# Optimization experiments

Hardware: AMD Instinct MI355X
Metric: run time of the kernel (lower is better)

## Reference

```python
import jax, jax.numpy as jnp
import numpy as np

B = 32768
T = 30
H = 384


def setup_inputs() -> dict:
    key = jax.random.key(0)
    ks = jax.random.split(key, 16)

    def lin(k, out_d, in_d):
        # torch nn.Linear init: U(-1/sqrt(in_d), 1/sqrt(in_d))
        bound = 1.0 / np.sqrt(in_d)
        kw, kb = jax.random.split(k)
        W = jax.random.uniform(kw, (out_d, in_d), jnp.float32, -bound, bound)
        b = jax.random.uniform(kb, (out_d,), jnp.float32, -bound, bound)
        return W, b

    Wp, bp = lin(ks[0], 128, 3)        # plan_input
    Ws, bs = lin(ks[1], 128, 3)        # state_input
    # GRUCell params: weight_ih [3H,128], weight_hh [3H,H], init U(-1/sqrt(H),..)
    gb = 1.0 / np.sqrt(H)
    W_ih = jax.random.uniform(ks[2], (3 * H, 128), jnp.float32, -gb, gb)
    b_ih = jax.random.uniform(ks[3], (3 * H,), jnp.float32, -gb, gb)
    W_hh = jax.random.uniform(ks[4], (3 * H, H), jnp.float32, -gb, gb)
    b_hh = jax.random.uniform(ks[5], (3 * H,), jnp.float32, -gb, gb)
    Wd1, bd1 = lin(ks[6], 64, H)       # decode Linear(384,64)
    Wd2, bd2 = lin(ks[7], 3, 64)       # decode Linear(64,3)

    init_hidden = jax.random.normal(ks[8], (B, H), jnp.float32)
    plan = jax.random.normal(ks[9], (B, T, 3), jnp.float32)
    gate = jax.random.uniform(ks[10], (B, 1), jnp.float32)
    init_state = jax.random.normal(ks[11], (B, 3), jnp.float32)

    return {
        "init_hidden": init_hidden, "plan": plan, "gate": gate,
        "init_state": init_state,
        "Wp": Wp, "bp": bp, "Ws": Ws, "bs": bs,
        "W_ih": W_ih, "b_ih": b_ih, "W_hh": W_hh, "b_hh": b_hh,
        "Wd1": Wd1, "bd1": bd1, "Wd2": Wd2, "bd2": bd2,
    }


def reference(init_hidden, plan, gate, init_state,
              Wp, bp, Ws, bs, W_ih, b_ih, W_hh, b_hh,
              Wd1, bd1, Wd2, bd2):
    # Dropout(0.1) is identity in eval mode.
    plan_seq = jnp.swapaxes(plan[:, :T, :3], 0, 1)  # [T,B,3]

    def step(carry, plan_t):
        hidden, state = carry  # [B,H], [B,3]
        x = (state @ Ws.T + bs) + (plan_t @ Wp.T + bp) * gate  # [B,128]
        gi = x @ W_ih.T + b_ih          # [B,3H]
        gh = hidden @ W_hh.T + b_hh     # [B,3H]
        ir, iz, inn = jnp.split(gi, 3, axis=-1)
        hr, hz, hn = jnp.split(gh, 3, axis=-1)
        r = jax.nn.sigmoid(ir + hr)
        z = jax.nn.sigmoid(iz + hz)
        n = jnp.tanh(inn + r * hn)
        hidden = (1.0 - z) * n + z * hidden
        dec = jax.nn.elu(hidden @ Wd1.T + bd1) @ Wd2.T + bd2  # [B,3]
        state = dec + state
        return (hidden, state), state

    _, outs = jax.lax.scan(step, (init_hidden, init_state[:, :3]), plan_seq)
    return jnp.swapaxes(outs, 0, 1)  # [B,T,3]
```

## Files before the change

### kernel.cpp

```cpp
#include <hip/hip_runtime.h>


#define TT  30
#define NPH 50
#define PHU 12288
#define HS  392

typedef unsigned short u16;
typedef __bf16 bf16x8 __attribute__((ext_vector_type(8)));
typedef u16    u16x8  __attribute__((ext_vector_type(8)));
typedef float  f32x16 __attribute__((ext_vector_type(16)));

__device__ __forceinline__ u16 f2b(float f){
  unsigned u = __float_as_uint(f);
  u += 0x7FFFu + ((u >> 16) & 1u);
  return (u16)(u >> 16);
}
__device__ __forceinline__ float b2f(u16 h){ return __uint_as_float(((unsigned)h) << 16); }

__device__ __forceinline__ f32x16 mfma32(u16x8 a, u16x8 b, f32x16 c){
  return __builtin_amdgcn_mfma_f32_32x32x16_bf16(
      __builtin_bit_cast(bf16x8, a), __builtin_bit_cast(bf16x8, b), c, 0, 0, 0);
}
__device__ __forceinline__ void lds_fence(){ asm volatile("s_waitcnt lgkmcnt(0)" ::: "memory"); }
__device__ __forceinline__ void vm_fence(){ asm volatile("s_waitcnt vmcnt(0)" ::: "memory"); }
__device__ __forceinline__ float sigf(float x){ return __builtin_amdgcn_rcpf(1.f + __expf(-x)); }
__device__ __forceinline__ float tanh_(float x){ return 2.f*__builtin_amdgcn_rcpf(1.f + __expf(-2.f*x)) - 1.f; }

__device__ __forceinline__ void stage16(const u16* g, u16* l){
  __builtin_amdgcn_global_load_lds(
      (const __attribute__((address_space(1))) unsigned int*)g,
      (__attribute__((address_space(3))) unsigned int*)l, 16, 0, 0);
}

__global__ void prep_kernel(const float* __restrict__ Wih, const float* __restrict__ Whh,
                            const float* __restrict__ Wd1, const float* __restrict__ Wd2,
                            const float* __restrict__ bih, const float* __restrict__ bhh,
                            const float* __restrict__ Ws,  const float* __restrict__ bs,
                            const float* __restrict__ Wp,  const float* __restrict__ bp,
                            u16* __restrict__ stream, u16* __restrict__ wd2p,
                            u16* __restrict__ wxp, float* __restrict__ gb)
{
  int i = blockIdx.x*blockDim.x + threadIdx.x;
  if (i < 442368){
    int row = i/384, k = i - row*384;
    int g = row/384, unit = row - g*384, c = unit>>5, lc = unit&31;
    int kf = k>>4, hl = (k>>3)&1, j = k&7;
    int phase = c*4 + 1 + g;
    stream[(size_t)phase*PHU + kf*512 + (lc+32*hl)*8 + j] = f2b(Whh[i]);
  }
  if (i < 147456){
    int row = i>>7, k = i&127;
    int g = row/384, unit = row - g*384, c = unit>>5, lc = unit&31;
    int kf = k>>4, hl = (k>>3)&1, j = k&7;
    int phase = c*4;
    stream[(size_t)phase*PHU + (g*8+kf)*512 + (lc+32*hl)*8 + j] = f2b(Wih[i]);
  }
  if (i < 24576){
    int row = i/384, k = i - row*384;
    int ct = row>>5, lc = row&31;
    int kf = k>>4, hl = (k>>3)&1, j = k&7;
    int phase = 48 + ct;
    stream[(size_t)phase*PHU + kf*512 + (lc+32*hl)*8 + j] = f2b(Wd1[i]);
  }
  if (i < 2048){
    int kf = i>>9, r = i&511;
    int n = (r>>3)&31, hl = r>>8, j = r&7;
    int k = kf*16 + hl*8 + j;
    wd2p[i] = f2b((n<3) ? Wd2[n*64 + k] : 0.f);
  }
  if (i < 2048){
    int tl = i>>9, r = i&511;
    int n = (r>>3)&31, hl = r>>8, j = r&7;
    int k = hl*8 + j, u = tl*32 + n;
    float v = 0.f;
    if      (k <= 2) v = Ws[u*3 + k];
    else if (k == 3) v = bs[u];
    else if (k <= 6) v = Wp[u*3 + (k-4)];
    else if (k == 7) v = bp[u];
    wxp[i] = f2b(v);
  }
  if (i < 384){
    gb[i*4+0] = bih[i]       + bhh[i];
    gb[i*4+1] = bih[384+i]   + bhh[384+i];
    gb[i*4+2] = bih[768+i];
    gb[i*4+3] = bhh[768+i];
  }
}

__global__ __launch_bounds__(256, 1)
void gru_main(const float* __restrict__ ih, const float* __restrict__ plan,
              const float* __restrict__ gate, const float* __restrict__ istate,
              const u16* __restrict__ stream, const u16* __restrict__ wd2p,
              const u16* __restrict__ wxp, const float* __restrict__ gb,
              const float* __restrict__ bd1, const float* __restrict__ bd2,
              float* __restrict__ out)
{
  __shared__ __attribute__((aligned(16))) u16 wb[2][PHU];
  __shared__ __attribute__((aligned(16))) u16 hn[4][32*HS];
  __shared__ float sst[4][32][4];

  const int tid  = threadIdx.x;
  const int wave = tid >> 6, lane = tid & 63;
  const int m    = lane & 31, hl = lane >> 5;
  const int R0   = blockIdx.x*128 + wave*32;
  u16* hw = hn[wave];

  const float gt    = gate[R0 + m];
  const float bd1v0 = bd1[m], bd1v1 = bd1[32+m];
  const float bd2v  = (m<3) ? bd2[m] : 0.f;

  if (lane < 32){
    const float* sp = istate + (size_t)(R0+lane)*3;
    sst[wave][lane][0]=sp[0]; sst[wave][lane][1]=sp[1];
    sst[wave][lane][2]=sp[2]; sst[wave][lane][3]=0.f;
  }

  u16x8 hold[24];
#pragma unroll
  for (int kf=0; kf<24; ++kf){
    const float* p = ih + (size_t)(R0+m)*384 + kf*16 + hl*8;
    float4 a = *(const float4*)p;
    float4 b = *(const float4*)(p+4);
    u16x8 v;
    v[0]=f2b(a.x); v[1]=f2b(a.y); v[2]=f2b(a.z); v[3]=f2b(a.w);
    v[4]=f2b(b.x); v[5]=f2b(b.y); v[6]=f2b(b.z); v[7]=f2b(b.w);
    hold[kf]=v;
    *(u16x8*)&hw[m*HS + kf*16 + hl*8] = v;
  }

  const u16* srcb = stream + wave*3072 + lane*8;
  auto stage = [&](int ph, int bsel){
    const u16* s = srcb + (size_t)ph*PHU;
    u16* d = &wb[bsel][wave*3072];
#pragma unroll
    for (int ii=0; ii<6; ++ii) stage16(s + ii*512, d + ii*512);
  };

  stage(0, 0);
  vm_fence(); __syncthreads();
  int buf = 0, gp = 0;

#pragma unroll 1
  for (int t=0; t<TT; ++t){
    u16x8 a8;
    {
      float4 sv = *(const float4*)&sst[wave][m][0];
      const float* pp = plan + (size_t)(R0+m)*(TT*3) + t*3;
      float f0=sv.x, f1=sv.y, f2=sv.z, f3=1.f;
      float f4=gt*pp[0], f5=gt*pp[1], f6=gt*pp[2], f7=gt;
      if (hl){ a8[0]=0;a8[1]=0;a8[2]=0;a8[3]=0;a8[4]=0;a8[5]=0;a8[6]=0;a8[7]=0; }
      else { a8[0]=f2b(f0);a8[1]=f2b(f1);a8[2]=f2b(f2);a8[3]=f2b(f3);
             a8[4]=f2b(f4);a8[5]=f2b(f5);a8[6]=f2b(f6);a8[7]=f2b(f7); }
    }
    u16x8 xf[8];
#pragma unroll
    for (int tl=0; tl<4; ++tl){
      f32x16 ax;
#pragma unroll
      for (int r=0;r<16;++r) ax[r]=0.f;
      ax = mfma32(a8, *(const u16x8*)(wxp + tl*512 + lane*8), ax);
#pragma unroll
      for (int r=0;r<16;++r){
        int row = (r&3) + ((r>>2)<<3) + 4*hl;
        hw[row*HS + m] = f2b(ax[r]);
      }
      lds_fence();
      xf[2*tl]   = *(const u16x8*)&hw[m*HS + hl*8];
      xf[2*tl+1] = *(const u16x8*)&hw[m*HS + 16 + hl*8];
      lds_fence();
    }
    *(u16x8*)&hw[m*HS + hl*8]      = hold[0];
    *(u16x8*)&hw[m*HS + 16 + hl*8] = hold[1];
    lds_fence();

#pragma unroll 1
    for (int c=0; c<12; ++c){
      f32x16 aR, aZ, aNI, aNH;
      {
        const float4 b4 = *(const float4*)(gb + (size_t)(c*32+m)*4);
#pragma unroll
        for (int r=0;r<16;++r){ aR[r]=b4.x; aZ[r]=b4.y; aNI[r]=b4.z; aNH[r]=b4.w; }
      }
      {
        int np = gp+1; stage(np, buf^1);
        const u16* W = wb[buf];
#pragma unroll
        for (int kf=0; kf<8; ++kf){
          u16x8 bR = *(const u16x8*)(W + (kf    )*512 + lane*8);
          u16x8 bZ = *(const u16x8*)(W + (8+kf  )*512 + lane*8);
          u16x8 bN = *(const u16x8*)(W + (16+kf )*512 + lane*8);
          aR  = mfma32(xf[kf], bR, aR);
          aZ  = mfma32(xf[kf], bZ, aZ);
          aNI = mfma32(xf[kf], bN, aNI);
        }
        vm_fence(); __syncthreads(); buf^=1; gp=np;
      }
      {
        int np = gp+1; stage(np, buf^1);
        const u16* W = wb[buf];
#pragma unroll
        for (int kf=0; kf<24; ++kf)
          aR = mfma32(hold[kf], *(const u16x8*)(W + kf*512 + lane*8), aR);
        vm_fence(); __syncthreads(); buf^=1; gp=np;
      }
      {
        int np = gp+1; stage(np, buf^1);
        const u16* W = wb[buf];
#pragma unroll
        for (int kf=0; kf<24; ++kf)
          aZ = mfma32(hold[kf], *(const u16x8*)(W + kf*512 + lane*8), aZ);
        vm_fence(); __syncthreads(); buf^=1; gp=np;
      }
      {
        int np = gp+1; stage(np, buf^1);
        const u16* W = wb[buf];
#pragma unroll
        for (int kf=0; kf<24; ++kf)
          aNH = mfma32(hold[kf], *(const u16x8*)(W + kf*512 + lane*8), aNH);
#pragma unroll
        for (int r=0;r<16;++r){
          int row = (r&3) + ((r>>2)<<3) + 4*hl;
          float rr = sigf(aR[r]);
          float zz = sigf(aZ[r]);
          float nn = tanh_(aNI[r] + rr*aNH[r]);
          int off = row*HS + c*32 + m;
          float ho = b2f(hw[off]);
          hw[off] = f2b((1.f-zz)*nn + zz*ho);
        }
        vm_fence(); __syncthreads(); buf^=1; gp=np;
      }
    }

    lds_fence();
#pragma unroll
    for (int kf=0; kf<24; ++kf)
      hold[kf] = *(const u16x8*)&hw[m*HS + kf*16 + hl*8];

    f32x16 a0, a1;
#pragma unroll
    for (int r=0;r<16;++r){ a0[r]=bd1v0; a1[r]=bd1v1; }
    {
      int np = gp+1; stage(np, buf^1);
      const u16* W = wb[buf];
#pragma unroll
      for (int kf=0; kf<24; ++kf)
        a0 = mfma32(hold[kf], *(const u16x8*)(W + kf*512 + lane*8), a0);
      vm_fence(); __syncthreads(); buf^=1; gp=np;
    }
    {
      int np = (gp+1 == NPH) ? 0 : gp+1;
      stage(np, buf^1);
      const u16* W = wb[buf];
#pragma unroll
      for (int kf=0; kf<24; ++kf)
        a1 = mfma32(hold[kf], *(const u16x8*)(W + kf*512 + lane*8), a1);

      u16x8 wd2f0 = *(const u16x8*)(wd2p + 0*512 + lane*8);
      u16x8 wd2f1 = *(const u16x8*)(wd2p + 1*512 + lane*8);
      u16x8 wd2f2 = *(const u16x8*)(wd2p + 2*512 + lane*8);
      u16x8 wd2f3 = *(const u16x8*)(wd2p + 3*512 + lane*8);

      f32x16 ao;
#pragma unroll
      for (int r=0;r<16;++r) ao[r]=0.f;
#pragma unroll
      for (int r=0;r<16;++r){
        int row = (r&3) + ((r>>2)<<3) + 4*hl;
        float e = a0[r]; e = e>0.f ? e : (__expf(e)-1.f);
        hw[row*HS + m] = f2b(e);
      }
      lds_fence();
      {
        u16x8 af0 = *(const u16x8*)&hw[m*HS + hl*8];
        u16x8 af1 = *(const u16x8*)&hw[m*HS + 16 + hl*8];
        ao = mfma32(af0, wd2f0, ao);
        ao = mfma32(af1, wd2f1, ao);
      }
      lds_fence();
#pragma unroll
      for (int r=0;r<16;++r){
        int row = (r&3) + ((r>>2)<<3) + 4*hl;
        float e = a1[r]; e = e>0.f ? e : (__expf(e)-1.f);
        hw[row*HS + m] = f2b(e);
      }
      lds_fence();
      {
        u16x8 af0 = *(const u16x8*)&hw[m*HS + hl*8];
        u16x8 af1 = *(const u16x8*)&hw[m*HS + 16 + hl*8];
        ao = mfma32(af0, wd2f2, ao);
        ao = mfma32(af1, wd2f3, ao);
      }
      lds_fence();
      *(u16x8*)&hw[m*HS + hl*8]      = hold[0];
      *(u16x8*)&hw[m*HS + 16 + hl*8] = hold[1];

#pragma unroll
      for (int r=0;r<16;++r){
        int row = (r&3) + ((r>>2)<<3) + 4*hl;
        if (m < 3){
          float ns = sst[wave][row][m] + ao[r] + bd2v;
          out[(size_t)(R0+row)*(TT*3) + t*3 + m] = ns;
          sst[wave][row][m] = ns;
        }
      }
      vm_fence(); __syncthreads(); buf^=1; gp=np;
    }
  }
}

extern "C" void kernel_launch(void* const* d_in, const int* in_sizes, int n_in,
                              void* d_out, int out_size, void* d_ws, size_t ws_size,
                              hipStream_t stream)
{
  (void)in_sizes; (void)n_in; (void)out_size; (void)ws_size;
  const float* ih     = (const float*)d_in[0];
  const float* plan   = (const float*)d_in[1];
  const float* gatep  = (const float*)d_in[2];
  const float* istate = (const float*)d_in[3];
  const float* Wp     = (const float*)d_in[4];
  const float* bp     = (const float*)d_in[5];
  const float* Ws     = (const float*)d_in[6];
  const float* bs     = (const float*)d_in[7];
  const float* Wih    = (const float*)d_in[8];
  const float* bih    = (const float*)d_in[9];
  const float* Whh    = (const float*)d_in[10];
  const float* bhh    = (const float*)d_in[11];
  const float* Wd1    = (const float*)d_in[12];
  const float* bd1    = (const float*)d_in[13];
  const float* Wd2    = (const float*)d_in[14];
  const float* bd2    = (const float*)d_in[15];

  u16*   wstream = (u16*)d_ws;
  u16*   wd2p    = (u16*)((char*)d_ws + 1228800);
  u16*   wxp     = (u16*)((char*)d_ws + 1232896);
  float* gb      = (float*)((char*)d_ws + 1236992);

  prep_kernel<<<1728, 256, 0, stream>>>(Wih, Whh, Wd1, Wd2, bih, bhh, Ws, bs, Wp, bp,
                                        wstream, wd2p, wxp, gb);
  gru_main<<<256, 256, 0, stream>>>(ih, plan, gatep, istate,
                                    wstream, wd2p, wxp, gb, bd1, bd2, (float*)d_out);
}
```

Baseline: 1.727 ms.

## Split hidden columns across wave pairs to double waves per block

Each group of 32 rows is now handled by a pair of waves, each computing half of the 384 hidden units, with the weight stream relaid into per-role half phases. Block size doubles to 512 threads so more waves hide MFMA and LDS latency, and per-wave work per phase is halved. The cost is twice as many block barriers per timestep and cross-wave exchange of hidden state and decode activations through LDS; register pressure under the new launch bounds may also rise.

```diff
diff --git a/kernel.cpp b/kernel.cpp
--- a/kernel.cpp
+++ b/kernel.cpp
@@ -2,8 +2,9 @@
 
 
 #define TT  30
-#define NPH 50
-#define PHU 12288
+#define NHP 50
+#define SPU 12288
+#define RHU 6144
 #define HS  392
 
 typedef unsigned short u16;
@@ -46,22 +47,27 @@
     int row = i/384, k = i - row*384;
     int g = row/384, unit = row - g*384, c = unit>>5, lc = unit&31;
     int kf = k>>4, hl = (k>>3)&1, j = k&7;
-    int phase = c*4 + 1 + g;
-    stream[(size_t)phase*PHU + kf*512 + (lc+32*hl)*8 + j] = f2b(Whh[i]);
+    int role = c/6, ci = c - role*6;
+    int q = ci*96 + 24 + g*24 + kf;
+    int sp = q/12, f = q - sp*12;
+    stream[(size_t)sp*SPU + role*RHU + f*512 + (lc+32*hl)*8 + j] = f2b(Whh[i]);
   }
   if (i < 147456){
     int row = i>>7, k = i&127;
     int g = row/384, unit = row - g*384, c = unit>>5, lc = unit&31;
     int kf = k>>4, hl = (k>>3)&1, j = k&7;
-    int phase = c*4;
-    stream[(size_t)phase*PHU + (g*8+kf)*512 + (lc+32*hl)*8 + j] = f2b(Wih[i]);
+    int role = c/6, ci = c - role*6;
+    int q = ci*96 + g*8 + kf;
+    int sp = q/12, f = q - sp*12;
+    stream[(size_t)sp*SPU + role*RHU + f*512 + (lc+32*hl)*8 + j] = f2b(Wih[i]);
   }
   if (i < 24576){
     int row = i/384, k = i - row*384;
     int ct = row>>5, lc = row&31;
     int kf = k>>4, hl = (k>>3)&1, j = k&7;
-    int phase = 48 + ct;
-    stream[(size_t)phase*PHU + kf*512 + (lc+32*hl)*8 + j] = f2b(Wd1[i]);
+    int q = 576 + kf;
+    int sp = q/12, f = q - sp*12;
+    stream[(size_t)sp*SPU + ct*RHU + f*512 + (lc+32*hl)*8 + j] = f2b(Wd1[i]);
   }
   if (i < 2048){
     int kf = i>>9, r = i&511;
@@ -88,7 +94,7 @@
   }
 }
 
-__global__ __launch_bounds__(256, 1)
+__global__ __launch_bounds__(512, 2)
 void gru_main(const float* __restrict__ ih, const float* __restrict__ plan,
               const float* __restrict__ gate, const float* __restrict__ istate,
               const u16* __restrict__ stream, const u16* __restrict__ wd2p,
@@ -96,24 +102,26 @@
               const float* __restrict__ bd1, const float* __restrict__ bd2,
               float* __restrict__ out)
 {
-  __shared__ __attribute__((aligned(16))) u16 wb[2][PHU];
+  __shared__ __attribute__((aligned(16))) u16 wb[2][SPU];
   __shared__ __attribute__((aligned(16))) u16 hn[4][32*HS];
   __shared__ float sst[4][32][4];
 
   const int tid  = threadIdx.x;
   const int wave = tid >> 6, lane = tid & 63;
+  const int pair = wave >> 1, role = wave & 1;
   const int m    = lane & 31, hl = lane >> 5;
-  const int R0   = blockIdx.x*128 + wave*32;
-  u16* hw = hn[wave];
-
-  const float gt    = gate[R0 + m];
-  const float bd1v0 = bd1[m], bd1v1 = bd1[32+m];
-  const float bd2v  = (m<3) ? bd2[m] : 0.f;
-
-  if (lane < 32){
+  const int R0   = blockIdx.x*128 + pair*32;
+  u16* hw = hn[pair];
+  const int scol = role*192;
+
+  const float gt   = gate[R0 + m];
+  const float bd1v = bd1[role*32 + m];
+  const float bd2v = (m<3) ? bd2[m] : 0.f;
+
+  if (role==0 && lane < 32){
     const float* sp = istate + (size_t)(R0+lane)*3;
-    sst[wave][lane][0]=sp[0]; sst[wave][lane][1]=sp[1];
-    sst[wave][lane][2]=sp[2]; sst[wave][lane][3]=0.f;
+    sst[pair][lane][0]=sp[0]; sst[pair][lane][1]=sp[1];
+    sst[pair][lane][2]=sp[2]; sst[pair][lane][3]=0.f;
   }
 
   u16x8 hold[24];
@@ -126,15 +134,15 @@
     v[0]=f2b(a.x); v[1]=f2b(a.y); v[2]=f2b(a.z); v[3]=f2b(a.w);
     v[4]=f2b(b.x); v[5]=f2b(b.y); v[6]=f2b(b.z); v[7]=f2b(b.w);
     hold[kf]=v;
-    *(u16x8*)&hw[m*HS + kf*16 + hl*8] = v;
-  }
-
-  const u16* srcb = stream + wave*3072 + lane*8;
-  auto stage = [&](int ph, int bsel){
-    const u16* s = srcb + (size_t)ph*PHU;
-    u16* d = &wb[bsel][wave*3072];
-#pragma unroll
-    for (int ii=0; ii<6; ++ii) stage16(s + ii*512, d + ii*512);
+    if (role==0) *(u16x8*)&hw[m*HS + kf*16 + hl*8] = v;
+  }
+
+  const u16* srcb = stream + wave*1536 + lane*8;
+  auto stage = [&](int sp, int bsel){
+    const u16* s = srcb + (size_t)sp*SPU;
+    u16* d = &wb[bsel][wave*1536];
+#pragma unroll
+    for (int ii=0; ii<3; ++ii) stage16(s + ii*512, d + ii*512);
   };
 
   stage(0, 0);
@@ -145,7 +153,7 @@
   for (int t=0; t<TT; ++t){
     u16x8 a8;
     {
-      float4 sv = *(const float4*)&sst[wave][m][0];
+      float4 sv = *(const float4*)&sst[pair][m][0];
       const float* pp = plan + (size_t)(R0+m)*(TT*3) + t*3;
       float f0=sv.x, f1=sv.y, f2=sv.z, f3=1.f;
       float f4=gt*pp[0], f5=gt*pp[1], f6=gt*pp[2], f7=gt;
@@ -163,68 +171,106 @@
 #pragma unroll
       for (int r=0;r<16;++r){
         int row = (r&3) + ((r>>2)<<3) + 4*hl;
-        hw[row*HS + m] = f2b(ax[r]);
+        hw[row*HS + scol + m] = f2b(ax[r]);
       }
       lds_fence();
-      xf[2*tl]   = *(const u16x8*)&hw[m*HS + hl*8];
-      xf[2*tl+1] = *(const u16x8*)&hw[m*HS + 16 + hl*8];
+      xf[2*tl]   = *(const u16x8*)&hw[m*HS + scol + hl*8];
+      xf[2*tl+1] = *(const u16x8*)&hw[m*HS + scol + 16 + hl*8];
       lds_fence();
     }
-    *(u16x8*)&hw[m*HS + hl*8]      = hold[0];
-    *(u16x8*)&hw[m*HS + 16 + hl*8] = hold[1];
+    if (role==0){
+      *(u16x8*)&hw[m*HS + hl*8]       = hold[0];
+      *(u16x8*)&hw[m*HS + 16 + hl*8]  = hold[1];
+    } else {
+      *(u16x8*)&hw[m*HS + 192 + hl*8] = hold[12];
+      *(u16x8*)&hw[m*HS + 208 + hl*8] = hold[13];
+    }
     lds_fence();
 
 #pragma unroll 1
-    for (int c=0; c<12; ++c){
+    for (int ci=0; ci<6; ++ci){
+      const int colb = scol + ci*32;
       f32x16 aR, aZ, aNI, aNH;
       {
-        const float4 b4 = *(const float4*)(gb + (size_t)(c*32+m)*4);
+        const float4 b4 = *(const float4*)(gb + (size_t)(colb+m)*4);
 #pragma unroll
         for (int r=0;r<16;++r){ aR[r]=b4.x; aZ[r]=b4.y; aNI[r]=b4.z; aNH[r]=b4.w; }
       }
       {
         int np = gp+1; stage(np, buf^1);
-        const u16* W = wb[buf];
-#pragma unroll
-        for (int kf=0; kf<8; ++kf){
-          u16x8 bR = *(const u16x8*)(W + (kf    )*512 + lane*8);
-          u16x8 bZ = *(const u16x8*)(W + (8+kf  )*512 + lane*8);
-          u16x8 bN = *(const u16x8*)(W + (16+kf )*512 + lane*8);
-          aR  = mfma32(xf[kf], bR, aR);
-          aZ  = mfma32(xf[kf], bZ, aZ);
-          aNI = mfma32(xf[kf], bN, aNI);
-        }
-        vm_fence(); __syncthreads(); buf^=1; gp=np;
-      }
-      {
-        int np = gp+1; stage(np, buf^1);
-        const u16* W = wb[buf];
-#pragma unroll
-        for (int kf=0; kf<24; ++kf)
+        const u16* W = wb[buf] + role*RHU;
+#pragma unroll
+        for (int kf=0; kf<8; ++kf)
+          aR = mfma32(xf[kf], *(const u16x8*)(W + kf*512 + lane*8), aR);
+#pragma unroll
+        for (int kf=0; kf<4; ++kf)
+          aZ = mfma32(xf[kf], *(const u16x8*)(W + (8+kf)*512 + lane*8), aZ);
+        vm_fence(); __syncthreads(); buf^=1; gp=np;
+      }
+      {
+        int np = gp+1; stage(np, buf^1);
+        const u16* W = wb[buf] + role*RHU;
+#pragma unroll
+        for (int kf=4; kf<8; ++kf)
+          aZ = mfma32(xf[kf], *(const u16x8*)(W + (kf-4)*512 + lane*8), aZ);
+#pragma unroll
+        for (int kf=0; kf<8; ++kf)
+          aNI = mfma32(xf[kf], *(const u16x8*)(W + (4+kf)*512 + lane*8), aNI);
+        vm_fence(); __syncthreads(); buf^=1; gp=np;
+      }
+      {
+        int np = gp+1; stage(np, buf^1);
+        const u16* W = wb[buf] + role*RHU;
+#pragma unroll
+        for (int kf=0; kf<12; ++kf)
           aR = mfma32(hold[kf], *(const u16x8*)(W + kf*512 + lane*8), aR);
         vm_fence(); __syncthreads(); buf^=1; gp=np;
       }
       {
         int np = gp+1; stage(np, buf^1);
-        const u16* W = wb[buf];
-#pragma unroll
-        for (int kf=0; kf<24; ++kf)
+        const u16* W = wb[buf] + role*RHU;
+#pragma unroll
+        for (int kk=0; kk<12; ++kk)
+          aR = mfma32(hold[12+kk], *(const u16x8*)(W + kk*512 + lane*8), aR);
+        vm_fence(); __syncthreads(); buf^=1; gp=np;
+      }
+      {
+        int np = gp+1; stage(np, buf^1);
+        const u16* W = wb[buf] + role*RHU;
+#pragma unroll
+        for (int kf=0; kf<12; ++kf)
           aZ = mfma32(hold[kf], *(const u16x8*)(W + kf*512 + lane*8), aZ);
         vm_fence(); __syncthreads(); buf^=1; gp=np;
       }
       {
         int np = gp+1; stage(np, buf^1);
-        const u16* W = wb[buf];
-#pragma unroll
-        for (int kf=0; kf<24; ++kf)
+        const u16* W = wb[buf] + role*RHU;
+#pragma unroll
+        for (int kk=0; kk<12; ++kk)
+          aZ = mfma32(hold[12+kk], *(const u16x8*)(W + kk*512 + lane*8), aZ);
+        vm_fence(); __syncthreads(); buf^=1; gp=np;
+      }
+      {
+        int np = gp+1; stage(np, buf^1);
+        const u16* W = wb[buf] + role*RHU;
+#pragma unroll
+        for (int kf=0; kf<12; ++kf)
           aNH = mfma32(hold[kf], *(const u16x8*)(W + kf*512 + lane*8), aNH);
+        vm_fence(); __syncthreads(); buf^=1; gp=np;
+      }
+      {
+        int np = gp+1; stage(np, buf^1);
+        const u16* W = wb[buf] + role*RHU;
+#pragma unroll
+        for (int kk=0; kk<12; ++kk)
+          aNH = mfma32(hold[12+kk], *(const u16x8*)(W + kk*512 + lane*8), aNH);
 #pragma unroll
         for (int r=0;r<16;++r){
           int row = (r&3) + ((r>>2)<<3) + 4*hl;
           float rr = sigf(aR[r]);
           float zz = sigf(aZ[r]);
           float nn = tanh_(aNI[r] + rr*aNH[r]);
-          int off = row*HS + c*32 + m;
+          int off = row*HS + colb + m;
           float ho = b2f(hw[off]);
           hw[off] = f2b((1.f-zz)*nn + zz*ho);
         }
@@ -232,79 +278,76 @@
       }
     }
 
-    lds_fence();
 #pragma unroll
     for (int kf=0; kf<24; ++kf)
       hold[kf] = *(const u16x8*)&hw[m*HS + kf*16 + hl*8];
 
-    f32x16 a0, a1;
-#pragma unroll
-    for (int r=0;r<16;++r){ a0[r]=bd1v0; a1[r]=bd1v1; }
+    f32x16 a0;
+#pragma unroll
+    for (int r=0;r<16;++r) a0[r]=bd1v;
     {
       int np = gp+1; stage(np, buf^1);
-      const u16* W = wb[buf];
-#pragma unroll
-      for (int kf=0; kf<24; ++kf)
+      const u16* W = wb[buf] + role*RHU;
+#pragma unroll
+      for (int kf=0; kf<12; ++kf)
         a0 = mfma32(hold[kf], *(const u16x8*)(W + kf*512 + lane*8), a0);
       vm_fence(); __syncthreads(); buf^=1; gp=np;
     }
     {
-      int np = (gp+1 == NPH) ? 0 : gp+1;
+      int np = (gp+1 == NHP) ? 0 : gp+1;
       stage(np, buf^1);
-      const u16* W = wb[buf];
-#pragma unroll
-      for (int kf=0; kf<24; ++kf)
-        a1 = mfma32(hold[kf], *(const u16x8*)(W + kf*512 + lane*8), a1);
-
+      const u16* W = wb[buf] + role*RHU;
+#pragma unroll
+      for (int kk=0; kk<12; ++kk)
+        a0 = mfma32(hold[12+kk], *(const u16x8*)(W + kk*512 + lane*8), a0);
+#pragma unroll
+      for (int r=0;r<16;++r){
+        int row = (r&3) + ((r>>2)<<3) + 4*hl;
+        float e = a0[r]; e = e>0.f ? e : (__expf(e)-1.f);
+        hw[row*HS + scol + m] = f2b(e);
+      }
+      vm_fence(); __syncthreads(); buf^=1; gp=np;
+    }
+    {
       u16x8 wd2f0 = *(const u16x8*)(wd2p + 0*512 + lane*8);
       u16x8 wd2f1 = *(const u16x8*)(wd2p + 1*512 + lane*8);
       u16x8 wd2f2 = *(const u16x8*)(wd2p + 2*512 + lane*8);
       u16x8 wd2f3 = *(const u16x8*)(wd2p + 3*512 + lane*8);
 
+      u16x8 af0 = *(const u16x8*)&hw[m*HS + hl*8];
+      u16x8 af1 = *(const u16x8*)&hw[m*HS + 16  + hl*8];
+      u16x8 af2 = *(const u16x8*)&hw[m*HS + 192 + hl*8];
+      u16x8 af3 = *(const u16x8*)&hw[m*HS + 208 + hl*8];
       f32x16 ao;
 #pragma unroll
       for (int r=0;r<16;++r) ao[r]=0.f;
-#pragma unroll
-      for (int r=0;r<16;++r){
-        int row = (r&3) + ((r>>2)<<3) + 4*hl;
-        float e = a0[r]; e = e>0.f ? e : (__expf(e)-1.f);
-        hw[row*HS + m] = f2b(e);
-      }
-      lds_fence();
-      {
-        u16x8 af0 = *(const u16x8*)&hw[m*HS + hl*8];
-        u16x8 af1 = *(const u16x8*)&hw[m*HS + 16 + hl*8];
-        ao = mfma32(af0, wd2f0, ao);
-        ao = mfma32(af1, wd2f1, ao);
-      }
-      lds_fence();
-#pragma unroll
-      for (int r=0;r<16;++r){
-        int row = (r&3) + ((r>>2)<<3) + 4*hl;
-        float e = a1[r]; e = e>0.f ? e : (__expf(e)-1.f);
-        hw[row*HS + m] = f2b(e);
-      }
-      lds_fence();
-      {
-        u16x8 af0 = *(const u16x8*)&hw[m*HS + hl*8];
-        u16x8 af1 = *(const u16x8*)&hw[m*HS + 16 + hl*8];
-        ao = mfma32(af0, wd2f2, ao);
-        ao = mfma32(af1, wd2f3, ao);
-      }
-      lds_fence();
-      *(u16x8*)&hw[m*HS + hl*8]      = hold[0];
-      *(u16x8*)&hw[m*HS + 16 + hl*8] = hold[1];
-
-#pragma unroll
-      for (int r=0;r<16;++r){
-        int row = (r&3) + ((r>>2)<<3) + 4*hl;
-        if (m < 3){
-          float ns = sst[wave][row][m] + ao[r] + bd2v;
-          out[(size_t)(R0+row)*(TT*3) + t*3 + m] = ns;
-          sst[wave][row][m] = ns;
+      ao = mfma32(af0, wd2f0, ao);
+      ao = mfma32(af1, wd2f1, ao);
+      ao = mfma32(af2, wd2f2, ao);
+      ao = mfma32(af3, wd2f3, ao);
+
+      __syncthreads();
+
+      if (role==0){
+        *(u16x8*)&hw[m*HS + hl*8]       = hold[0];
+        *(u16x8*)&hw[m*HS + 16 + hl*8]  = hold[1];
+      } else {
+        *(u16x8*)&hw[m*HS + 192 + hl*8] = hold[12];
+        *(u16x8*)&hw[m*HS + 208 + hl*8] = hold[13];
+      }
+
+      if (role==0){
+#pragma unroll
+        for (int r=0;r<16;++r){
+          int row = (r&3) + ((r>>2)<<3) + 4*hl;
+          if (m < 3){
+            float ns = sst[pair][row][m] + ao[r] + bd2v;
+            out[(size_t)(R0+row)*(TT*3) + t*3 + m] = ns;
+            sst[pair][row][m] = ns;
+          }
         }
       }
-      vm_fence(); __syncthreads(); buf^=1; gp=np;
+      __syncthreads();
     }
   }
 }
@@ -338,6 +381,6 @@
 
   prep_kernel<<<1728, 256, 0, stream>>>(Wih, Whh, Wd1, Wd2, bih, bhh, Ws, bs, Wp, bp,
                                         wstream, wd2p, wxp, gb);
-  gru_main<<<256, 256, 0, stream>>>(ih, plan, gatep, istate,
+  gru_main<<<256, 512, 0, stream>>>(ih, plan, gatep, istate,
                                     wstream, wd2p, wxp, gb, bd1, bd2, (float*)d_out);
 }
```

After: 1.950 ms. 1.13x slower.

## Deepen weight staging to a five-slot half-phase ring with partial vmcnt waits

Applied to the files above, without the earlier changes.

Replaces the double-buffered full-phase LDS weight staging with a ring of five half-phase slots. The loads for upcoming phases run further ahead, and each phase boundary waits with vmcnt(3) instead of draining all global loads, so load latency can overlap the MFMA work. The running state is moved into padding columns of the per-wave hidden buffer, and sched_barriers are added around the fences. The cost is more complex slot indexing and stricter dependence on exact load-count ordering, where a mismatch would give wrong results.

```diff
diff --git a/kernel.cpp b/kernel.cpp
--- a/kernel.cpp
+++ b/kernel.cpp
@@ -4,6 +4,8 @@
 #define TT  30
 #define NPH 50
 #define PHU 12288
+#define HPU 6144
+#define STRU 614400
 #define HS  392
 
 typedef unsigned short u16;
@@ -22,8 +24,10 @@
   return __builtin_amdgcn_mfma_f32_32x32x16_bf16(
       __builtin_bit_cast(bf16x8, a), __builtin_bit_cast(bf16x8, b), c, 0, 0, 0);
 }
-__device__ __forceinline__ void lds_fence(){ asm volatile("s_waitcnt lgkmcnt(0)" ::: "memory"); }
-__device__ __forceinline__ void vm_fence(){ asm volatile("s_waitcnt vmcnt(0)" ::: "memory"); }
+__device__ __forceinline__ void lds_fence(){
+  asm volatile("s_waitcnt lgkmcnt(0)" ::: "memory");
+  __builtin_amdgcn_sched_barrier(0);
+}
 __device__ __forceinline__ float sigf(float x){ return __builtin_amdgcn_rcpf(1.f + __expf(-x)); }
 __device__ __forceinline__ float tanh_(float x){ return 2.f*__builtin_amdgcn_rcpf(1.f + __expf(-2.f*x)) - 1.f; }
 
@@ -96,9 +100,8 @@
               const float* __restrict__ bd1, const float* __restrict__ bd2,
               float* __restrict__ out)
 {
-  __shared__ __attribute__((aligned(16))) u16 wb[2][PHU];
+  __shared__ __attribute__((aligned(16))) u16 wb[5*HPU];
   __shared__ __attribute__((aligned(16))) u16 hn[4][32*HS];
-  __shared__ float sst[4][32][4];
 
   const int tid  = threadIdx.x;
   const int wave = tid >> 6, lane = tid & 63;
@@ -112,8 +115,8 @@
 
   if (lane < 32){
     const float* sp = istate + (size_t)(R0+lane)*3;
-    sst[wave][lane][0]=sp[0]; sst[wave][lane][1]=sp[1];
-    sst[wave][lane][2]=sp[2]; sst[wave][lane][3]=0.f;
+    float* q = (float*)&hw[lane*HS + 384];
+    q[0]=sp[0]; q[1]=sp[1]; q[2]=sp[2]; q[3]=0.f;
   }
 
   u16x8 hold[24];
@@ -129,23 +132,38 @@
     *(u16x8*)&hw[m*HS + kf*16 + hl*8] = v;
   }
 
-  const u16* srcb = stream + wave*3072 + lane*8;
-  auto stage = [&](int ph, int bsel){
-    const u16* s = srcb + (size_t)ph*PHU;
-    u16* d = &wb[bsel][wave*3072];
-#pragma unroll
-    for (int ii=0; ii<6; ++ii) stage16(s + ii*512, d + ii*512);
+  int hoff = 0;
+  int ss   = 0;
+  int sa   = 0, sb = 1;
+  auto stage_half = [&](){
+    const u16* s = stream + hoff + wave*1536 + lane*8;
+    u16* d = &wb[ss*HPU + wave*1536];
+    stage16(s,        d);
+    stage16(s + 512,  d + 512);
+    stage16(s + 1024, d + 1024);
+    hoff += HPU; if (hoff == STRU) hoff = 0;
+    ss = (ss==4) ? 0 : ss+1;
   };
-
-  stage(0, 0);
-  vm_fence(); __syncthreads();
-  int buf = 0, gp = 0;
+  auto phase_end = [&](){
+    asm volatile("s_waitcnt vmcnt(3) lgkmcnt(0)" ::: "memory");
+    __builtin_amdgcn_sched_barrier(0);
+    __builtin_amdgcn_s_barrier();
+    __builtin_amdgcn_sched_barrier(0);
+    sa = (sa>=3) ? sa-3 : sa+2;
+    sb = (sb>=3) ? sb-3 : sb+2;
+  };
+
+  stage_half(); stage_half(); stage_half();
+  asm volatile("s_waitcnt vmcnt(3) lgkmcnt(0)" ::: "memory");
+  __builtin_amdgcn_sched_barrier(0);
+  __builtin_amdgcn_s_barrier();
+  __builtin_amdgcn_sched_barrier(0);
 
 #pragma unroll 1
   for (int t=0; t<TT; ++t){
     u16x8 a8;
     {
-      float4 sv = *(const float4*)&sst[wave][m][0];
+      float4 sv = *(const float4*)&hw[m*HS + 384];
       const float* pp = plan + (size_t)(R0+m)*(TT*3) + t*3;
       float f0=sv.x, f1=sv.y, f2=sv.z, f3=1.f;
       float f4=gt*pp[0], f5=gt*pp[1], f6=gt*pp[2], f7=gt;
@@ -183,41 +201,51 @@
         for (int r=0;r<16;++r){ aR[r]=b4.x; aZ[r]=b4.y; aNI[r]=b4.z; aNH[r]=b4.w; }
       }
       {
-        int np = gp+1; stage(np, buf^1);
-        const u16* W = wb[buf];
+        stage_half(); stage_half();
+        const u16* W0 = wb + sa*HPU;
+        const u16* W1 = wb + sb*HPU;
 #pragma unroll
         for (int kf=0; kf<8; ++kf){
-          u16x8 bR = *(const u16x8*)(W + (kf    )*512 + lane*8);
-          u16x8 bZ = *(const u16x8*)(W + (8+kf  )*512 + lane*8);
-          u16x8 bN = *(const u16x8*)(W + (16+kf )*512 + lane*8);
-          aR  = mfma32(xf[kf], bR, aR);
-          aZ  = mfma32(xf[kf], bZ, aZ);
-          aNI = mfma32(xf[kf], bN, aNI);
-        }
-        vm_fence(); __syncthreads(); buf^=1; gp=np;
-      }
-      {
-        int np = gp+1; stage(np, buf^1);
-        const u16* W = wb[buf];
-#pragma unroll
-        for (int kf=0; kf<24; ++kf)
-          aR = mfma32(hold[kf], *(const u16x8*)(W + kf*512 + lane*8), aR);
-        vm_fence(); __syncthreads(); buf^=1; gp=np;
-      }
-      {
-        int np = gp+1; stage(np, buf^1);
-        const u16* W = wb[buf];
-#pragma unroll
-        for (int kf=0; kf<24; ++kf)
-          aZ = mfma32(hold[kf], *(const u16x8*)(W + kf*512 + lane*8), aZ);
-        vm_fence(); __syncthreads(); buf^=1; gp=np;
-      }
-      {
-        int np = gp+1; stage(np, buf^1);
-        const u16* W = wb[buf];
-#pragma unroll
-        for (int kf=0; kf<24; ++kf)
-          aNH = mfma32(hold[kf], *(const u16x8*)(W + kf*512 + lane*8), aNH);
+          const u16* bR = W0 + kf*512;
+          const u16* bZ = (kf<4) ? W0 + (8+kf)*512 : W1 + (kf-4)*512;
+          const u16* bN = W1 + (4+kf)*512;
+          aR  = mfma32(xf[kf], *(const u16x8*)(bR + lane*8), aR);
+          aZ  = mfma32(xf[kf], *(const u16x8*)(bZ + lane*8), aZ);
+          aNI = mfma32(xf[kf], *(const u16x8*)(bN + lane*8), aNI);
+        }
+        phase_end();
+      }
+      {
+        stage_half(); stage_half();
+        const u16* W0 = wb + sa*HPU;
+        const u16* W1 = wb + sb*HPU;
+#pragma unroll
+        for (int kf=0; kf<24; ++kf){
+          const u16* Bp = (kf<12) ? W0 + kf*512 : W1 + (kf-12)*512;
+          aR = mfma32(hold[kf], *(const u16x8*)(Bp + lane*8), aR);
+        }
+        phase_end();
+      }
+      {
+        stage_half(); stage_half();
+        const u16* W0 = wb + sa*HPU;
+        const u16* W1 = wb + sb*HPU;
+#pragma unroll
+        for (int kf=0; kf<24; ++kf){
+          const u16* Bp = (kf<12) ? W0 + kf*512 : W1 + (kf-12)*512;
+          aZ = mfma32(hold[kf], *(const u16x8*)(Bp + lane*8), aZ);
+        }
+        phase_end();
+      }
+      {
+        stage_half(); stage_half();
+        const u16* W0 = wb + sa*HPU;
+        const u16* W1 = wb + sb*HPU;
+#pragma unroll
+        for (int kf=0; kf<24; ++kf){
+          const u16* Bp = (kf<12) ? W0 + kf*512 : W1 + (kf-12)*512;
+          aNH = mfma32(hold[kf], *(const u16x8*)(Bp + lane*8), aNH);
+        }
 #pragma unroll
         for (int r=0;r<16;++r){
           int row = (r&3) + ((r>>2)<<3) + 4*hl;
@@ -228,7 +256,7 @@
           float ho = b2f(hw[off]);
           hw[off] = f2b((1.f-zz)*nn + zz*ho);
         }
-        vm_fence(); __syncthreads(); buf^=1; gp=np;
+        phase_end();
       }
     }
 
@@ -241,20 +269,25 @@
 #pragma unroll
     for (int r=0;r<16;++r){ a0[r]=bd1v0; a1[r]=bd1v1; }
     {
-      int np = gp+1; stage(np, buf^1);
-      const u16* W = wb[buf];
-#pragma unroll
-      for (int kf=0; kf<24; ++kf)
-        a0 = mfma32(hold[kf], *(const u16x8*)(W + kf*512 + lane*8), a0);
-      vm_fence(); __syncthreads(); buf^=1; gp=np;
+      stage_half(); stage_half();
+      const u16* W0 = wb + sa*HPU;
+      const u16* W1 = wb + sb*HPU;
+#pragma unroll
+      for (int kf=0; kf<24; ++kf){
+        const u16* Bp = (kf<12) ? W0 + kf*512 : W1 + (kf-12)*512;
+        a0 = mfma32(hold[kf], *(const u16x8*)(Bp + lane*8), a0);
+      }
+      phase_end();
     }
     {
-      int np = (gp+1 == NPH) ? 0 : gp+1;
-      stage(np, buf^1);
-      const u16* W = wb[buf];
-#pragma unroll
-      for (int kf=0; kf<24; ++kf)
-        a1 = mfma32(hold[kf], *(const u16x8*)(W + kf*512 + lane*8), a1);
+      stage_half(); stage_half();
+      const u16* W0 = wb + sa*HPU;
+      const u16* W1 = wb + sb*HPU;
+#pragma unroll
+      for (int kf=0; kf<24; ++kf){
+        const u16* Bp = (kf<12) ? W0 + kf*512 : W1 + (kf-12)*512;
+        a1 = mfma32(hold[kf], *(const u16x8*)(Bp + lane*8), a1);
+      }
 
       u16x8 wd2f0 = *(const u16x8*)(wd2p + 0*512 + lane*8);
       u16x8 wd2f1 = *(const u16x8*)(wd2p + 1*512 + lane*8);
@@ -299,12 +332,13 @@
       for (int r=0;r<16;++r){
         int row = (r&3) + ((r>>2)<<3) + 4*hl;
         if (m < 3){
-          float ns = sst[wave][row][m] + ao[r] + bd2v;
+          float* q = (float*)&hw[row*HS + 384];
+          float ns = q[m] + ao[r] + bd2v;
           out[(size_t)(R0+row)*(TT*3) + t*3 + m] = ns;
-          sst[wave][row][m] = ns;
-        }
-      }
-      vm_fence(); __syncthreads(); buf^=1; gp=np;
+          q[m] = ns;
+        }
+      }
+      phase_end();
     }
   }
 }
```

Result: no change. 1.719 ms (-0.5%).

## Split hidden units across waves with 32-row blocks and shared streamed weights

Applied to the files above, without the earlier changes.

Each block now handles 32 batch rows instead of 128, and its four waves split the 12 hidden-unit chunks (and the decode halves) among themselves instead of each wave covering all units for its own rows. The weight stream is reorganised into smaller 8K-element phases, with each wave staging its own slice, and 1024 blocks are launched with two blocks per CU allowed. The aim is more parallelism and occupancy from a smaller LDS footprint. The cost is far more block-wide barriers per step, and each block now streams the full weight set for only 32 rows, which quadruples total weight traffic.

```diff
diff --git a/kernel.cpp b/kernel.cpp
--- a/kernel.cpp
+++ b/kernel.cpp
@@ -1,10 +1,11 @@
 #include <hip/hip_runtime.h>
 
 
-#define TT  30
-#define NPH 50
-#define PHU 12288
-#define HS  392
+#define TT   30
+#define NPH  75
+#define SPU  8192
+#define HS   392
+#define XFO(kf,hh,mm) (((kf)*2+(hh))*264 + (mm)*8)
 
 typedef unsigned short u16;
 typedef __bf16 bf16x8 __attribute__((ext_vector_type(8)));
@@ -46,22 +47,29 @@
     int row = i/384, k = i - row*384;
     int g = row/384, unit = row - g*384, c = unit>>5, lc = unit&31;
     int kf = k>>4, hl = (k>>3)&1, j = k&7;
-    int phase = c*4 + 1 + g;
-    stream[(size_t)phase*PHU + kf*512 + (lc+32*hl)*8 + j] = f2b(Whh[i]);
+    int role = c/3, ci = c - role*3;
+    int q = ci*96 + 24 + g*24 + kf;
+    int sp = q>>2, f = q&3;
+    stream[(size_t)sp*SPU + role*2048 + f*512 + (lc+32*hl)*8 + j] = f2b(Whh[i]);
   }
   if (i < 147456){
     int row = i>>7, k = i&127;
     int g = row/384, unit = row - g*384, c = unit>>5, lc = unit&31;
     int kf = k>>4, hl = (k>>3)&1, j = k&7;
-    int phase = c*4;
-    stream[(size_t)phase*PHU + (g*8+kf)*512 + (lc+32*hl)*8 + j] = f2b(Wih[i]);
+    int role = c/3, ci = c - role*3;
+    int q = ci*96 + g*8 + kf;
+    int sp = q>>2, f = q&3;
+    stream[(size_t)sp*SPU + role*2048 + f*512 + (lc+32*hl)*8 + j] = f2b(Wih[i]);
   }
   if (i < 24576){
     int row = i/384, k = i - row*384;
-    int ct = row>>5, lc = row&31;
+    int tl = row>>5, lc = row&31;
     int kf = k>>4, hl = (k>>3)&1, j = k&7;
-    int phase = 48 + ct;
-    stream[(size_t)phase*PHU + kf*512 + (lc+32*hl)*8 + j] = f2b(Wd1[i]);
+    int kh = kf/12, kfp = kf - kh*12;
+    int role = tl*2 + kh;
+    int q = 288 + kfp;
+    int sp = q>>2, f = q&3;
+    stream[(size_t)sp*SPU + role*2048 + f*512 + (lc+32*hl)*8 + j] = f2b(Wd1[i]);
   }
   if (i < 2048){
     int kf = i>>9, r = i&511;
@@ -88,7 +96,7 @@
   }
 }
 
-__global__ __launch_bounds__(256, 1)
+__global__ __launch_bounds__(256, 2)
 void gru_main(const float* __restrict__ ih, const float* __restrict__ plan,
               const float* __restrict__ gate, const float* __restrict__ istate,
               const u16* __restrict__ stream, const u16* __restrict__ wd2p,
@@ -96,24 +104,24 @@
               const float* __restrict__ bd1, const float* __restrict__ bd2,
               float* __restrict__ out)
 {
-  __shared__ __attribute__((aligned(16))) u16 wb[2][PHU];
-  __shared__ __attribute__((aligned(16))) u16 hn[4][32*HS];
-  __shared__ float sst[4][32][4];
+  __shared__ __attribute__((aligned(16))) u16 wb[2][SPU];
+  __shared__ __attribute__((aligned(16))) u16 hn[32*HS];
+  __shared__ __attribute__((aligned(16))) u16 xsc[16*264];
+  __shared__ float scr[2][32*33];
 
   const int tid  = threadIdx.x;
   const int wave = tid >> 6, lane = tid & 63;
   const int m    = lane & 31, hl = lane >> 5;
-  const int R0   = blockIdx.x*128 + wave*32;
-  u16* hw = hn[wave];
-
-  const float gt    = gate[R0 + m];
-  const float bd1v0 = bd1[m], bd1v1 = bd1[32+m];
-  const float bd2v  = (m<3) ? bd2[m] : 0.f;
-
-  if (lane < 32){
+  const int R0   = blockIdx.x*32;
+
+  const float gt   = gate[R0 + m];
+  const float bd1v = (wave&1) ? 0.f : bd1[(wave>>1)*32 + m];
+  const float bd2v = (m<3) ? bd2[m] : 0.f;
+
+  if (wave==0 && lane < 32){
     const float* sp = istate + (size_t)(R0+lane)*3;
-    sst[wave][lane][0]=sp[0]; sst[wave][lane][1]=sp[1];
-    sst[wave][lane][2]=sp[2]; sst[wave][lane][3]=0.f;
+    float* q = (float*)&hn[lane*HS + 384];
+    q[0]=sp[0]; q[1]=sp[1]; q[2]=sp[2]; q[3]=0.f;
   }
 
   u16x8 hold[24];
@@ -126,15 +134,15 @@
     v[0]=f2b(a.x); v[1]=f2b(a.y); v[2]=f2b(a.z); v[3]=f2b(a.w);
     v[4]=f2b(b.x); v[5]=f2b(b.y); v[6]=f2b(b.z); v[7]=f2b(b.w);
     hold[kf]=v;
-    *(u16x8*)&hw[m*HS + kf*16 + hl*8] = v;
-  }
-
-  const u16* srcb = stream + wave*3072 + lane*8;
-  auto stage = [&](int ph, int bsel){
-    const u16* s = srcb + (size_t)ph*PHU;
-    u16* d = &wb[bsel][wave*3072];
-#pragma unroll
-    for (int ii=0; ii<6; ++ii) stage16(s + ii*512, d + ii*512);
+    if (wave==0) *(u16x8*)&hn[m*HS + kf*16 + hl*8] = v;
+  }
+
+  const u16* srcb = stream + wave*2048 + lane*8;
+  auto stage = [&](int sp, int bsel){
+    const u16* s = srcb + (size_t)sp*SPU;
+    u16* d = &wb[bsel][wave*2048];
+#pragma unroll
+    for (int ii=0; ii<4; ++ii) stage16(s + ii*512, d + ii*512);
   };
 
   stage(0, 0);
@@ -145,7 +153,7 @@
   for (int t=0; t<TT; ++t){
     u16x8 a8;
     {
-      float4 sv = *(const float4*)&sst[wave][m][0];
+      float4 sv = *(const float4*)&hn[m*HS + 384];
       const float* pp = plan + (size_t)(R0+m)*(TT*3) + t*3;
       float f0=sv.x, f1=sv.y, f2=sv.z, f3=1.f;
       float f4=gt*pp[0], f5=gt*pp[1], f6=gt*pp[2], f7=gt;
@@ -153,159 +161,148 @@
       else { a8[0]=f2b(f0);a8[1]=f2b(f1);a8[2]=f2b(f2);a8[3]=f2b(f3);
              a8[4]=f2b(f4);a8[5]=f2b(f5);a8[6]=f2b(f6);a8[7]=f2b(f7); }
     }
-    u16x8 xf[8];
-#pragma unroll
-    for (int tl=0; tl<4; ++tl){
+    {
       f32x16 ax;
 #pragma unroll
       for (int r=0;r<16;++r) ax[r]=0.f;
-      ax = mfma32(a8, *(const u16x8*)(wxp + tl*512 + lane*8), ax);
+      ax = mfma32(a8, *(const u16x8*)(wxp + wave*512 + lane*8), ax);
 #pragma unroll
       for (int r=0;r<16;++r){
         int row = (r&3) + ((r>>2)<<3) + 4*hl;
-        hw[row*HS + m] = f2b(ax[r]);
-      }
-      lds_fence();
-      xf[2*tl]   = *(const u16x8*)&hw[m*HS + hl*8];
-      xf[2*tl+1] = *(const u16x8*)&hw[m*HS + 16 + hl*8];
-      lds_fence();
-    }
-    *(u16x8*)&hw[m*HS + hl*8]      = hold[0];
-    *(u16x8*)&hw[m*HS + 16 + hl*8] = hold[1];
+        int kfx = 2*wave + (m>>4);
+        xsc[(kfx*2 + ((m>>3)&1))*264 + row*8 + (m&7)] = f2b(ax[r]);
+      }
+    }
+    __syncthreads();
+    u16x8 xf[8];
+#pragma unroll
+    for (int kf=0; kf<8; ++kf) xf[kf] = *(const u16x8*)&xsc[XFO(kf,hl,m)];
     lds_fence();
 
 #pragma unroll 1
-    for (int c=0; c<12; ++c){
+    for (int ci=0; ci<3; ++ci){
+      const int c = 3*wave + ci;
       f32x16 aR, aZ, aNI, aNH;
       {
         const float4 b4 = *(const float4*)(gb + (size_t)(c*32+m)*4);
 #pragma unroll
         for (int r=0;r<16;++r){ aR[r]=b4.x; aZ[r]=b4.y; aNI[r]=b4.z; aNH[r]=b4.w; }
       }
-      {
+#pragma unroll
+      for (int pg=0; pg<6; ++pg){
         int np = gp+1; stage(np, buf^1);
-        const u16* W = wb[buf];
-#pragma unroll
-        for (int kf=0; kf<8; ++kf){
-          u16x8 bR = *(const u16x8*)(W + (kf    )*512 + lane*8);
-          u16x8 bZ = *(const u16x8*)(W + (8+kf  )*512 + lane*8);
-          u16x8 bN = *(const u16x8*)(W + (16+kf )*512 + lane*8);
-          aR  = mfma32(xf[kf], bR, aR);
-          aZ  = mfma32(xf[kf], bZ, aZ);
-          aNI = mfma32(xf[kf], bN, aNI);
+        const u16* W = wb[buf] + wave*2048;
+#pragma unroll
+        for (int s=0; s<4; ++s){
+          int idx = pg*4+s, g = idx>>3, kf = idx&7;
+          u16x8 B = *(const u16x8*)(W + s*512 + lane*8);
+          if      (g==0) aR  = mfma32(xf[kf], B, aR);
+          else if (g==1) aZ  = mfma32(xf[kf], B, aZ);
+          else           aNI = mfma32(xf[kf], B, aNI);
         }
         vm_fence(); __syncthreads(); buf^=1; gp=np;
       }
-      {
+#pragma unroll
+      for (int pp=0; pp<18; ++pp){
         int np = gp+1; stage(np, buf^1);
-        const u16* W = wb[buf];
-#pragma unroll
-        for (int kf=0; kf<24; ++kf)
-          aR = mfma32(hold[kf], *(const u16x8*)(W + kf*512 + lane*8), aR);
-        vm_fence(); __syncthreads(); buf^=1; gp=np;
-      }
-      {
-        int np = gp+1; stage(np, buf^1);
-        const u16* W = wb[buf];
-#pragma unroll
-        for (int kf=0; kf<24; ++kf)
-          aZ = mfma32(hold[kf], *(const u16x8*)(W + kf*512 + lane*8), aZ);
-        vm_fence(); __syncthreads(); buf^=1; gp=np;
-      }
-      {
-        int np = gp+1; stage(np, buf^1);
-        const u16* W = wb[buf];
-#pragma unroll
-        for (int kf=0; kf<24; ++kf)
-          aNH = mfma32(hold[kf], *(const u16x8*)(W + kf*512 + lane*8), aNH);
-#pragma unroll
-        for (int r=0;r<16;++r){
-          int row = (r&3) + ((r>>2)<<3) + 4*hl;
-          float rr = sigf(aR[r]);
-          float zz = sigf(aZ[r]);
-          float nn = tanh_(aNI[r] + rr*aNH[r]);
-          int off = row*HS + c*32 + m;
-          float ho = b2f(hw[off]);
-          hw[off] = f2b((1.f-zz)*nn + zz*ho);
+        const u16* W = wb[buf] + wave*2048;
+#pragma unroll
+        for (int s=0; s<4; ++s){
+          int idx = pp*4+s, g = idx/24, kf = idx - g*24;
+          u16x8 B = *(const u16x8*)(W + s*512 + lane*8);
+          if      (g==0) aR  = mfma32(hold[kf], B, aR);
+          else if (g==1) aZ  = mfma32(hold[kf], B, aZ);
+          else           aNH = mfma32(hold[kf], B, aNH);
+        }
+        if (pp==17){
+#pragma unroll
+          for (int r=0;r<16;++r){
+            int row = (r&3) + ((r>>2)<<3) + 4*hl;
+            float rr = sigf(aR[r]);
+            float zz = sigf(aZ[r]);
+            float nn = tanh_(aNI[r] + rr*aNH[r]);
+            int off = row*HS + c*32 + m;
+            float ho = b2f(hn[off]);
+            hn[off] = f2b((1.f-zz)*nn + zz*ho);
+          }
         }
         vm_fence(); __syncthreads(); buf^=1; gp=np;
       }
     }
 
-    lds_fence();
 #pragma unroll
     for (int kf=0; kf<24; ++kf)
-      hold[kf] = *(const u16x8*)&hw[m*HS + kf*16 + hl*8];
-
-    f32x16 a0, a1;
-#pragma unroll
-    for (int r=0;r<16;++r){ a0[r]=bd1v0; a1[r]=bd1v1; }
-    {
-      int np = gp+1; stage(np, buf^1);
-      const u16* W = wb[buf];
-#pragma unroll
-      for (int kf=0; kf<24; ++kf)
-        a0 = mfma32(hold[kf], *(const u16x8*)(W + kf*512 + lane*8), a0);
-      vm_fence(); __syncthreads(); buf^=1; gp=np;
-    }
-    {
+      hold[kf] = *(const u16x8*)&hn[m*HS + kf*16 + hl*8];
+
+    f32x16 a0;
+#pragma unroll
+    for (int r=0;r<16;++r) a0[r]=bd1v;
+#pragma unroll
+    for (int pd=0; pd<3; ++pd){
       int np = (gp+1 == NPH) ? 0 : gp+1;
       stage(np, buf^1);
-      const u16* W = wb[buf];
-#pragma unroll
-      for (int kf=0; kf<24; ++kf)
-        a1 = mfma32(hold[kf], *(const u16x8*)(W + kf*512 + lane*8), a1);
-
+      const u16* W = wb[buf] + wave*2048;
+      if (wave & 1){
+#pragma unroll
+        for (int s=0; s<4; ++s)
+          a0 = mfma32(hold[12 + pd*4+s], *(const u16x8*)(W + s*512 + lane*8), a0);
+      } else {
+#pragma unroll
+        for (int s=0; s<4; ++s)
+          a0 = mfma32(hold[pd*4+s], *(const u16x8*)(W + s*512 + lane*8), a0);
+      }
+      vm_fence(); __syncthreads(); buf^=1; gp=np;
+    }
+    if (wave & 1){
+      float* sp_ = scr[wave>>1];
+#pragma unroll
+      for (int r=0;r<16;++r){
+        int row = (r&3) + ((r>>2)<<3) + 4*hl;
+        sp_[row*33 + m] = a0[r];
+      }
+    }
+    __syncthreads();
+    if (!(wave & 1)){
+      const float* sp_ = scr[wave>>1];
+      const int kb = (wave==0) ? 0 : 2;
+#pragma unroll
+      for (int r=0;r<16;++r){
+        int row = (r&3) + ((r>>2)<<3) + 4*hl;
+        float e = a0[r] + sp_[row*33 + m];
+        e = e>0.f ? e : (__expf(e)-1.f);
+        int kfd = kb + (m>>4);
+        xsc[(kfd*2 + ((m>>3)&1))*264 + row*8 + (m&7)] = f2b(e);
+      }
+    }
+    __syncthreads();
+    if (wave==0){
       u16x8 wd2f0 = *(const u16x8*)(wd2p + 0*512 + lane*8);
       u16x8 wd2f1 = *(const u16x8*)(wd2p + 1*512 + lane*8);
       u16x8 wd2f2 = *(const u16x8*)(wd2p + 2*512 + lane*8);
       u16x8 wd2f3 = *(const u16x8*)(wd2p + 3*512 + lane*8);
-
+      u16x8 af0 = *(const u16x8*)&xsc[XFO(0,hl,m)];
+      u16x8 af1 = *(const u16x8*)&xsc[XFO(1,hl,m)];
+      u16x8 af2 = *(const u16x8*)&xsc[XFO(2,hl,m)];
+      u16x8 af3 = *(const u16x8*)&xsc[XFO(3,hl,m)];
       f32x16 ao;
 #pragma unroll
       for (int r=0;r<16;++r) ao[r]=0.f;
-#pragma unroll
-      for (int r=0;r<16;++r){
-        int row = (r&3) + ((r>>2)<<3) + 4*hl;
-        float e = a0[r]; e = e>0.f ? e : (__expf(e)-1.f);
-        hw[row*HS + m] = f2b(e);
-      }
-      lds_fence();
-      {
-        u16x8 af0 = *(const u16x8*)&hw[m*HS + hl*8];
-        u16x8 af1 = *(const u16x8*)&hw[m*HS + 16 + hl*8];
-        ao = mfma32(af0, wd2f0, ao);
-        ao = mfma32(af1, wd2f1, ao);
-      }
-      lds_fence();
-#pragma unroll
-      for (int r=0;r<16;++r){
-        int row = (r&3) + ((r>>2)<<3) + 4*hl;
-        float e = a1[r]; e = e>0.f ? e : (__expf(e)-1.f);
-        hw[row*HS + m] = f2b(e);
-      }
-      lds_fence();
-      {
-        u16x8 af0 = *(const u16x8*)&hw[m*HS + hl*8];
-        u16x8 af1 = *(const u16x8*)&hw[m*HS + 16 + hl*8];
-        ao = mfma32(af0, wd2f2, ao);
-        ao = mfma32(af1, wd2f3, ao);
-      }
-      lds_fence();
-      *(u16x8*)&hw[m*HS + hl*8]      = hold[0];
-      *(u16x8*)&hw[m*HS + 16 + hl*8] = hold[1];
-
+      ao = mfma32(af0, wd2f0, ao);
+      ao = mfma32(af1, wd2f1, ao);
+      ao = mfma32(af2, wd2f2, ao);
+      ao = mfma32(af3, wd2f3, ao);
 #pragma unroll
       for (int r=0;r<16;++r){
         int row = (r&3) + ((r>>2)<<3) + 4*hl;
         if (m < 3){
-          float ns = sst[wave][row][m] + ao[r] + bd2v;
+          float* q = (float*)&hn[row*HS + 384];
+          float ns = q[m] + ao[r] + bd2v;
           out[(size_t)(R0+row)*(TT*3) + t*3 + m] = ns;
-          sst[wave][row][m] = ns;
+          q[m] = ns;
         }
       }
-      vm_fence(); __syncthreads(); buf^=1; gp=np;
-    }
+    }
+    __syncthreads();
   }
 }
 
@@ -338,6 +335,6 @@
 
   prep_kernel<<<1728, 256, 0, stream>>>(Wih, Whh, Wd1, Wd2, bih, bhh, Ws, bs, Wp, bp,
                                         wstream, wd2p, wxp, gb);
-  gru_main<<<256, 256, 0, stream>>>(ih, plan, gatep, istate,
-                                    wstream, wd2p, wxp, gb, bd1, bd2, (float*)d_out);
-}
+  gru_main<<<1024, 256, 0, stream>>>(ih, plan, gatep, istate,
+                                     wstream, wd2p, wxp, gb, bd1, bd2, (float*)d_out);
+}
```

Result: slower. 2.864 ms (+65.8%).
